# Performance work log

Measured on AMD Instinct MI355X. Metric: run time of the kernel, lower is better.

The kernel has to match this reference:

```python
import jax, jax.numpy as jnp
import numpy as np

BATCH_SIZE = 16384
TEMPERATURE = 0.5
EPS = 1e-8  # torch CosineSimilarity default eps


def setup_inputs() -> dict:
    key = jax.random.key(0)
    k1, k2 = jax.random.split(key)
    z_i = jax.random.normal(k1, (BATCH_SIZE, 512), dtype=jnp.float32)
    z_j = jax.random.normal(k2, (BATCH_SIZE, 512), dtype=jnp.float32)
    return {"z_i": z_i, "z_j": z_j}


def reference(z_i, z_j):
    # The torch module builds a full [2B, 2B] cosine-sim matrix and extracts
    # the +B and -B diagonals. Those diagonals are both cos(z_i[k], z_j[k]),
    # so we compute the row-wise cosine directly (identical math).
    B = z_i.shape[0]
    N = 2 * B
    dot = jnp.sum(z_i * z_j, axis=-1)                      # [B]
    norm_prod = jnp.linalg.norm(z_i, axis=-1) * jnp.linalg.norm(z_j, axis=-1)
    cos = dot / jnp.maximum(norm_prod, EPS)                # [B]
    pos = cos / TEMPERATURE                                # sim_i_j == sim_j_i
    # positive_samples = concat(sim_i_j, sim_j_i) -> 2B values, labels = 0
    # MSELoss(mean) = sum(pos^2) / (2B); then loss /= N
    mse = jnp.sum(jnp.square(pos)) * 2.0 / N
    loss = mse / N
    return loss
```

## Files before the change

### kernel.cpp

```cpp
#include <hip/hip_runtime.h>


constexpr int   B_ROWS = 16384;
constexpr int   D_DIM  = 512;
constexpr float EPS    = 1e-8f;
constexpr float INV_TEMP = 2.0f;
constexpr float SCALE    = 2.0f / (32768.0f * 32768.0f);

__global__ __launch_bounds__(256) void ntxent_pos_loss_kernel(
    const float* __restrict__ zi,
    const float* __restrict__ zj,
    float* __restrict__ out)
{
    const int lane        = threadIdx.x & 63;
    const int wave_in_blk = threadIdx.x >> 6;
    const int wave        = blockIdx.x * 4 + wave_in_blk;
    const int nwaves      = gridDim.x * 4;

    float acc = 0.0f;

    for (int row = wave; row < B_ROWS; row += nwaves) {
        const float4* a4 = (const float4*)(zi + (size_t)row * D_DIM);
        const float4* b4 = (const float4*)(zj + (size_t)row * D_DIM);

        float4 a0 = a4[lane];
        float4 a1 = a4[lane + 64];
        float4 b0 = b4[lane];
        float4 b1 = b4[lane + 64];

        float dot = a0.x * b0.x + a0.y * b0.y + a0.z * b0.z + a0.w * b0.w
                  + a1.x * b1.x + a1.y * b1.y + a1.z * b1.z + a1.w * b1.w;
        float na  = a0.x * a0.x + a0.y * a0.y + a0.z * a0.z + a0.w * a0.w
                  + a1.x * a1.x + a1.y * a1.y + a1.z * a1.z + a1.w * a1.w;
        float nb  = b0.x * b0.x + b0.y * b0.y + b0.z * b0.z + b0.w * b0.w
                  + b1.x * b1.x + b1.y * b1.y + b1.z * b1.z + b1.w * b1.w;

        #pragma unroll
        for (int off = 32; off > 0; off >>= 1) {
            dot += __shfl_down(dot, off, 64);
            na  += __shfl_down(na,  off, 64);
            nb  += __shfl_down(nb,  off, 64);
        }

        if (lane == 0) {
            float norm_prod = sqrtf(na) * sqrtf(nb);
            float cosv = dot / fmaxf(norm_prod, EPS);
            float pos  = cosv * INV_TEMP;
            acc += pos * pos;
        }
    }

    __shared__ float s[4];
    if (lane == 0) s[wave_in_blk] = acc;
    __syncthreads();
    if (threadIdx.x == 0) {
        float t = (s[0] + s[1]) + (s[2] + s[3]);
        atomicAdd(out, t * SCALE);
    }
}

extern "C" void kernel_launch(void* const* d_in, const int* in_sizes, int n_in,
                              void* d_out, int out_size, void* d_ws, size_t ws_size,
                              hipStream_t stream)
{
    const float* zi = (const float*)d_in[0];
    const float* zj = (const float*)d_in[1];
    float* out = (float*)d_out;

    hipMemsetAsync(out, 0, sizeof(float), stream);

    ntxent_pos_loss_kernel<<<2048, 256, 0, stream>>>(zi, zj, out);
}
```

Baseline: 112.9 us.

## Map one row per 16-lane group and replace atomics with two-stage reduction

Result: faster. 92.32 us (-18.2%).

```diff
diff --git a/kernel.cpp b/kernel.cpp
--- a/kernel.cpp
+++ b/kernel.cpp
@@ -1,62 +1,77 @@
 #include <hip/hip_runtime.h>
 
 
-constexpr int   B_ROWS = 16384;
 constexpr int   D_DIM  = 512;
 constexpr float EPS    = 1e-8f;
 constexpr float INV_TEMP = 2.0f;
 constexpr float SCALE    = 2.0f / (32768.0f * 32768.0f);
 
-__global__ __launch_bounds__(256) void ntxent_pos_loss_kernel(
+__global__ __launch_bounds__(256) void ntxent_partial_kernel(
     const float* __restrict__ zi,
     const float* __restrict__ zj,
-    float* __restrict__ out)
+    float* __restrict__ partials)
 {
     const int lane        = threadIdx.x & 63;
     const int wave_in_blk = threadIdx.x >> 6;
-    const int wave        = blockIdx.x * 4 + wave_in_blk;
-    const int nwaves      = gridDim.x * 4;
+    const int g    = lane & 15;
+    const int grp  = lane >> 4;
+    const int wave = blockIdx.x * 4 + wave_in_blk;
+    const int row  = wave * 4 + grp;
+
+    const float4* a4 = (const float4*)(zi + (size_t)row * D_DIM);
+    const float4* b4 = (const float4*)(zj + (size_t)row * D_DIM);
+
+    float dot = 0.0f, na = 0.0f, nb = 0.0f;
+    #pragma unroll
+    for (int k = 0; k < 8; ++k) {
+        float4 a = a4[g + 16 * k];
+        float4 b = b4[g + 16 * k];
+        dot += a.x * b.x + a.y * b.y + a.z * b.z + a.w * b.w;
+        na  += a.x * a.x + a.y * a.y + a.z * a.z + a.w * a.w;
+        nb  += b.x * b.x + b.y * b.y + b.z * b.z + b.w * b.w;
+    }
+
+    #pragma unroll
+    for (int m = 8; m >= 1; m >>= 1) {
+        dot += __shfl_xor(dot, m, 64);
+        na  += __shfl_xor(na,  m, 64);
+        nb  += __shfl_xor(nb,  m, 64);
+    }
 
     float acc = 0.0f;
-
-    for (int row = wave; row < B_ROWS; row += nwaves) {
-        const float4* a4 = (const float4*)(zi + (size_t)row * D_DIM);
-        const float4* b4 = (const float4*)(zj + (size_t)row * D_DIM);
-
-        float4 a0 = a4[lane];
-        float4 a1 = a4[lane + 64];
-        float4 b0 = b4[lane];
-        float4 b1 = b4[lane + 64];
-
-        float dot = a0.x * b0.x + a0.y * b0.y + a0.z * b0.z + a0.w * b0.w
-                  + a1.x * b1.x + a1.y * b1.y + a1.z * b1.z + a1.w * b1.w;
-        float na  = a0.x * a0.x + a0.y * a0.y + a0.z * a0.z + a0.w * a0.w
-                  + a1.x * a1.x + a1.y * a1.y + a1.z * a1.z + a1.w * a1.w;
-        float nb  = b0.x * b0.x + b0.y * b0.y + b0.z * b0.z + b0.w * b0.w
-                  + b1.x * b1.x + b1.y * b1.y + b1.z * b1.z + b1.w * b1.w;
-
-        #pragma unroll
-        for (int off = 32; off > 0; off >>= 1) {
-            dot += __shfl_down(dot, off, 64);
-            na  += __shfl_down(na,  off, 64);
-            nb  += __shfl_down(nb,  off, 64);
-        }
-
-        if (lane == 0) {
-            float norm_prod = sqrtf(na) * sqrtf(nb);
-            float cosv = dot / fmaxf(norm_prod, EPS);
-            float pos  = cosv * INV_TEMP;
-            acc += pos * pos;
-        }
+    if (g == 0) {
+        float norm_prod = sqrtf(na) * sqrtf(nb);
+        float cosv = dot / fmaxf(norm_prod, EPS);
+        float pos  = cosv * INV_TEMP;
+        acc = pos * pos;
     }
+    acc += __shfl_xor(acc, 16, 64);
+    acc += __shfl_xor(acc, 32, 64);
 
     __shared__ float s[4];
     if (lane == 0) s[wave_in_blk] = acc;
     __syncthreads();
-    if (threadIdx.x == 0) {
-        float t = (s[0] + s[1]) + (s[2] + s[3]);
-        atomicAdd(out, t * SCALE);
-    }
+    if (threadIdx.x == 0)
+        partials[blockIdx.x] = (s[0] + s[1]) + (s[2] + s[3]);
+}
+
+__global__ __launch_bounds__(256) void ntxent_finalize_kernel(
+    const float* __restrict__ partials,
+    float* __restrict__ out)
+{
+    float v = partials[threadIdx.x]
+            + partials[threadIdx.x + 256]
+            + partials[threadIdx.x + 512]
+            + partials[threadIdx.x + 768];
+    #pragma unroll
+    for (int m = 32; m >= 1; m >>= 1)
+        v += __shfl_xor(v, m, 64);
+
+    __shared__ float s[4];
+    if ((threadIdx.x & 63) == 0) s[threadIdx.x >> 6] = v;
+    __syncthreads();
+    if (threadIdx.x == 0)
+        out[0] = ((s[0] + s[1]) + (s[2] + s[3])) * SCALE;
 }
 
 extern "C" void kernel_launch(void* const* d_in, const int* in_sizes, int n_in,
@@ -65,9 +80,9 @@
 {
     const float* zi = (const float*)d_in[0];
     const float* zj = (const float*)d_in[1];
+    float* partials = (float*)d_ws;
     float* out = (float*)d_out;
 
-    hipMemsetAsync(out, 0, sizeof(float), stream);
-
-    ntxent_pos_loss_kernel<<<2048, 256, 0, stream>>>(zi, zj, out);
+    ntxent_partial_kernel<<<1024, 256, 0, stream>>>(zi, zj, partials);
+    ntxent_finalize_kernel<<<1, 256, 0, stream>>>(partials, out);
 }
```
